# Performance work log

Measured on AMD Instinct MI355X. Metric: run time of the kernel, lower is better.

The kernel has to match this reference:

```python
import jax, jax.numpy as jnp
import numpy as np

B, S, D, H = 2, 2048, 1024, 16
DH = D // H  # 64


def setup_inputs() -> dict:
    key = jax.random.key(0)
    ks = jax.random.split(key, 9)
    s = 1.0 / np.sqrt(D)
    return {
        "x": jax.random.normal(ks[0], (B, S, D), dtype=jnp.float32),
        "Wq": jax.random.normal(ks[1], (D, D), dtype=jnp.float32) * s,
        "bq": jnp.zeros((D,), dtype=jnp.float32),
        "Wk": jax.random.normal(ks[2], (D, D), dtype=jnp.float32) * s,
        "bk": jnp.zeros((D,), dtype=jnp.float32),
        "Wv": jax.random.normal(ks[3], (D, D), dtype=jnp.float32) * s,
        "bv": jnp.zeros((D,), dtype=jnp.float32),
        "Wo": jax.random.normal(ks[4], (D, D), dtype=jnp.float32) * s,
        "bo": jnp.zeros((D,), dtype=jnp.float32),
    }


def _split_heads(t):
    # [B, S, D] -> [B, H, S, DH]
    return t.reshape(B, S, H, DH).transpose(0, 2, 1, 3)


def reference(x, Wq, bq, Wk, bk, Wv, bv, Wo, bo):
    q = _split_heads(x @ Wq + bq)
    k = _split_heads(x @ Wk + bk)
    v = _split_heads(x @ Wv + bv)
    scale = 1.0 / jnp.sqrt(jnp.asarray(DH, dtype=x.dtype))
    # [B, H, S, S] score matrix (materialized, as in the original)
    logits = jnp.einsum("bhqd,bhkd->bhqk", q, k) * scale
    attn = jax.nn.softmax(logits, axis=-1)
    out = jnp.einsum("bhqk,bhkd->bhqd", attn, v)
    out = out.transpose(0, 2, 1, 3).reshape(B, S, D)
    return out @ Wo + bo
```

## Files before the change

kernel.cpp:

```cpp
#include <hip/hip_runtime.h>
#include <hip/hip_bf16.h>
#include <stdint.h>


typedef __attribute__((ext_vector_type(8))) short bf16x8;
typedef __attribute__((ext_vector_type(4))) float f32x4;

__device__ __forceinline__ void gld16(const void* g, void* l) {
  __builtin_amdgcn_global_load_lds((const __attribute__((address_space(1))) void*)g,
                                   (__attribute__((address_space(3))) void*)l, 16, 0, 0);
}

__device__ __forceinline__ unsigned short f2b(float f) {
  __hip_bfloat16 h = __float2bfloat16(f);
  return *reinterpret_cast<unsigned short*>(&h);
}

__global__ __launch_bounds__(256) void prep_kernel(const float* __restrict__ x,
                                                   const float* __restrict__ Wq,
                                                   const float* __restrict__ Wk,
                                                   const float* __restrict__ Wv,
                                                   const float* __restrict__ Wo,
                                                   unsigned short* __restrict__ xb,
                                                   unsigned short* __restrict__ wt) {
  __shared__ unsigned short Ls[64 * 72];
  int bid = blockIdx.x;
  int t = threadIdx.x;
  if (bid < 4096) {
    int i = (bid * 256 + t) * 4;
    float4 v = *(const float4*)(x + i);
    ushort4 o = make_ushort4(f2b(v.x), f2b(v.y), f2b(v.z), f2b(v.w));
    *(ushort4*)(xb + i) = o;
    return;
  }
  int tid = bid - 4096;
  int z = tid >> 8, rem = tid & 255;
  int bx = rem & 15, by = rem >> 4;
  const float* src = (z == 0) ? Wq : (z == 1) ? Wk : (z == 2) ? Wv : Wo;
  unsigned short* dst = wt + (size_t)z * 1024 * 1024;
  int k0 = bx * 64, n0 = by * 64;
  int c4 = t & 15;
#pragma unroll
  for (int it = 0; it < 4; ++it) {
    int row = it * 16 + (t >> 4);
    float4 v = *(const float4*)(src + (k0 + row) * 1024 + n0 + c4 * 4);
    Ls[(c4 * 4 + 0) * 72 + row] = f2b(v.x);
    Ls[(c4 * 4 + 1) * 72 + row] = f2b(v.y);
    Ls[(c4 * 4 + 2) * 72 + row] = f2b(v.z);
    Ls[(c4 * 4 + 3) * 72 + row] = f2b(v.w);
  }
  __syncthreads();
  int nr = t >> 2, kc = (t & 3) * 16;
  *(uint4*)(dst + (size_t)(n0 + nr) * 1024 + k0 + kc) = *(uint4*)&Ls[nr * 72 + kc];
  *(uint4*)(dst + (size_t)(n0 + nr) * 1024 + k0 + kc + 8) = *(uint4*)&Ls[nr * 72 + kc + 8];
}

__global__ __launch_bounds__(256) void gemm_qkv(const unsigned short* __restrict__ Ab,
                                                const unsigned short* __restrict__ Bt,
                                                const float* __restrict__ bq,
                                                const float* __restrict__ bk,
                                                const float* __restrict__ bv,
                                                unsigned short* __restrict__ qb,
                                                unsigned short* __restrict__ kb,
                                                unsigned short* __restrict__ vtb) {
  __shared__ unsigned short As[128 * 32];
  __shared__ unsigned short Bs[128 * 32];
  __shared__ unsigned short Es[128 * 72];
  const int t = threadIdx.x;
  const int lane = t & 63, wave = t >> 6;
  const int m0 = blockIdx.x * 128, n0 = blockIdx.y * 128;
  const int wr = (wave >> 1) * 64, wc = (wave & 1) * 64;
  const int fr = lane & 15, fq = lane >> 4;
  f32x4 acc[4][4] = {};
  for (int kt = 0; kt < 32; ++kt) {
    const unsigned short* Ag = Ab + (size_t)m0 * 1024 + kt * 32;
    const unsigned short* Bg = Bt + (size_t)n0 * 1024 + kt * 32;
#pragma unroll
    for (int rep = 0; rep < 2; ++rep) {
      int c = t + rep * 256;
      int row = c >> 2, col = (c & 3) * 8;
      gld16(Ag + (size_t)row * 1024 + col, (void*)(As + c * 8));
      gld16(Bg + (size_t)row * 1024 + col, (void*)(Bs + c * 8));
    }
    __syncthreads();
    bf16x8 a[4], b[4];
#pragma unroll
    for (int i = 0; i < 4; ++i) a[i] = *(const bf16x8*)&As[(wr + i * 16 + fr) * 32 + fq * 8];
#pragma unroll
    for (int j = 0; j < 4; ++j) b[j] = *(const bf16x8*)&Bs[(wc + j * 16 + fr) * 32 + fq * 8];
#pragma unroll
    for (int i = 0; i < 4; ++i)
#pragma unroll
      for (int j = 0; j < 4; ++j)
        acc[i][j] = __builtin_amdgcn_mfma_f32_16x16x32_bf16(a[i], b[j], acc[i][j], 0, 0, 0);
    __syncthreads();
  }
  const int which = n0 >> 10;
  const int bidx = m0 >> 11, s0 = m0 & 2047;
  if (which == 2) {
#pragma unroll
    for (int nh = 0; nh < 2; ++nh) {
      if ((wc >> 6) == nh) {
#pragma unroll
        for (int j = 0; j < 4; ++j) {
          int col = j * 16 + fr;
          float bias = bv[(n0 + nh * 64 + col) & 1023];
#pragma unroll
          for (int i = 0; i < 4; ++i) {
            int sl = wr + i * 16 + fq * 4;
            ushort4 pk;
            pk.x = f2b(acc[i][j][0] + bias);
            pk.y = f2b(acc[i][j][1] + bias);
            pk.z = f2b(acc[i][j][2] + bias);
            pk.w = f2b(acc[i][j][3] + bias);
            *(uint2*)&Es[col * 136 + sl] = *(uint2*)&pk;
          }
        }
      }
      __syncthreads();
      int h = ((n0 + nh * 64) & 1023) >> 6;
#pragma unroll
      for (int it = 0; it < 4; ++it) {
        int dh = it * 16 + (t >> 4);
        int ck = (t & 15) * 8;
        uint4 vv = *(uint4*)&Es[dh * 136 + ck];
        *(uint4*)&vtb[(size_t)((bidx * 16 + h) * 64 + dh) * 2048 + s0 + ck] = vv;
      }
      __syncthreads();
    }
  } else {
    unsigned short* dst = (which == 0) ? qb : kb;
    const float* bias_p = (which == 0) ? bq : bk;
    float scale = (which == 0) ? 0.1803368801111204f : 1.0f;
#pragma unroll
    for (int nh = 0; nh < 2; ++nh) {
      if ((wc >> 6) == nh) {
#pragma unroll
        for (int j = 0; j < 4; ++j) {
          int col = j * 16 + fr;
          float bias = bias_p[(n0 + nh * 64 + col) & 1023];
#pragma unroll
          for (int i = 0; i < 4; ++i)
#pragma unroll
            for (int r = 0; r < 4; ++r) {
              int sl = wr + i * 16 + fq * 4 + r;
              Es[sl * 72 + col] = f2b((acc[i][j][r] + bias) * scale);
            }
        }
      }
      __syncthreads();
      int h = ((n0 + nh * 64) & 1023) >> 6;
#pragma unroll
      for (int it = 0; it < 4; ++it) {
        int sl = it * 32 + (t >> 3);
        int ck = (t & 7) * 8;
        uint4 vv = *(uint4*)&Es[sl * 72 + ck];
        *(uint4*)&dst[(size_t)((bidx * 16 + h) * 2048 + s0 + sl) * 64 + ck] = vv;
      }
      __syncthreads();
    }
  }
}

__global__ __launch_bounds__(256, 2) void attn_kernel(const unsigned short* __restrict__ qb,
                                                      const unsigned short* __restrict__ kb,
                                                      const unsigned short* __restrict__ vtb,
                                                      unsigned short* __restrict__ attn) {
  __shared__ unsigned short Ks[2 * 4096];
  __shared__ unsigned short Vs[2 * 4096];
  __shared__ unsigned short Ps[4 * 2048];
  const int t = threadIdx.x, lane = t & 63, w = t >> 6;
  const int fr = lane & 15, fq = lane >> 4;
  const int rid = blockIdx.y * 16 + blockIdx.x;
  const int bh = (rid & 7) + ((rid >> 7) << 3);
  const int q0 = ((rid >> 3) & 15) * 128;
  const int ksel = (fq ^ ((fr >> 1) & 3)) * 8;
  const unsigned short* qg = qb + (size_t)bh * 2048 * 64;
  const unsigned short* kg0 = kb + (size_t)bh * 2048 * 64;
  const unsigned short* vg0 = vtb + (size_t)bh * 64 * 2048;

  bf16x8 qf[2][2];
#pragma unroll
  for (int nb = 0; nb < 2; ++nb)
#pragma unroll
    for (int kk = 0; kk < 2; ++kk)
      qf[nb][kk] = *(const bf16x8*)(qg + (size_t)(q0 + w * 32 + nb * 16 + fr) * 64 + kk * 32 + fq * 8);

  bf16x8 ones;
#pragma unroll
  for (int i = 0; i < 8; ++i) ones[i] = (short)0x3F80;

  f32x4 oacc[2][4] = {};
  f32x4 lacc[2] = {};
  unsigned short* Pw = Ps + w * 2048;

  {
#pragma unroll
    for (int rep = 0; rep < 2; ++rep) {
      int c = t + rep * 256;
      int kk = c >> 8, row = (c >> 2) & 63, cc = c & 3;
      int cs = cc ^ ((row >> 1) & 3);
      gld16(kg0 + row * 64 + kk * 32 + cs * 8, (void*)(Ks + c * 8));
      gld16(vg0 + (size_t)row * 2048 + kk * 32 + cs * 8, (void*)(Vs + c * 8));
    }
  }

  for (int kt = 0; kt < 32; ++kt) {
    int buf = kt & 1;
    __syncthreads();
    if (kt + 1 < 32) {
      const unsigned short* kg = kg0 + (size_t)(kt + 1) * 4096;
      const unsigned short* vg = vg0 + (kt + 1) * 64;
      int lb = (buf ^ 1) * 4096;
#pragma unroll
      for (int rep = 0; rep < 2; ++rep) {
        int c = t + rep * 256;
        int kk = c >> 8, row = (c >> 2) & 63, cc = c & 3;
        int cs = cc ^ ((row >> 1) & 3);
        gld16(kg + row * 64 + kk * 32 + cs * 8, (void*)(Ks + lb + c * 8));
        gld16(vg + (size_t)row * 2048 + kk * 32 + cs * 8, (void*)(Vs + lb + c * 8));
      }
    }
    const unsigned short* Kb = Ks + buf * 4096;
    const unsigned short* Vb = Vs + buf * 4096;
    f32x4 sacc[4][2] = {};
#pragma unroll
    for (int kk = 0; kk < 2; ++kk) {
      bf16x8 kf[4];
#pragma unroll
      for (int m = 0; m < 4; ++m) kf[m] = *(const bf16x8*)&Kb[kk * 2048 + (m * 16 + fr) * 32 + ksel];
      __builtin_amdgcn_s_setprio(1);
#pragma unroll
      for (int m = 0; m < 4; ++m)
#pragma unroll
        for (int nb = 0; nb < 2; ++nb)
          sacc[m][nb] = __builtin_amdgcn_mfma_f32_16x16x32_bf16(kf[m], qf[nb][kk], sacc[m][nb], 0, 0, 0);
      __builtin_amdgcn_s_setprio(0);
    }
#pragma unroll
    for (int m = 0; m < 4; ++m)
#pragma unroll
      for (int nb = 0; nb < 2; ++nb) {
        int qw = nb * 16 + fr;
        int G = (m * 2 + (fq >> 1)) ^ (qw & 7);
        ushort4 pk;
        pk.x = f2b(__builtin_amdgcn_exp2f(sacc[m][nb][0]));
        pk.y = f2b(__builtin_amdgcn_exp2f(sacc[m][nb][1]));
        pk.z = f2b(__builtin_amdgcn_exp2f(sacc[m][nb][2]));
        pk.w = f2b(__builtin_amdgcn_exp2f(sacc[m][nb][3]));
        *(uint2*)&Pw[qw * 64 + G * 8 + (fq & 1) * 4] = *(uint2*)&pk;
      }
#pragma unroll
    for (int kk = 0; kk < 2; ++kk) {
      bf16x8 pf[2];
#pragma unroll
      for (int mb = 0; mb < 2; ++mb) {
        int qw = mb * 16 + fr;
        int G = (kk * 4 + fq) ^ (qw & 7);
        pf[mb] = *(const bf16x8*)&Pw[qw * 64 + G * 8];
      }
      __builtin_amdgcn_s_setprio(1);
#pragma unroll
      for (int n = 0; n < 4; ++n) {
        bf16x8 vf = *(const bf16x8*)&Vb[kk * 2048 + (n * 16 + fr) * 32 + ksel];
#pragma unroll
        for (int mb = 0; mb < 2; ++mb)
          oacc[mb][n] = __builtin_amdgcn_mfma_f32_16x16x32_bf16(pf[mb], vf, oacc[mb][n], 0, 0, 0);
      }
#pragma unroll
      for (int mb = 0; mb < 2; ++mb)
        lacc[mb] = __builtin_amdgcn_mfma_f32_16x16x32_bf16(pf[mb], ones, lacc[mb], 0, 0, 0);
      __builtin_amdgcn_s_setprio(0);
    }
  }
  int bidx = bh >> 4, h = bh & 15;
#pragma unroll
  for (int mb = 0; mb < 2; ++mb)
#pragma unroll
    for (int r = 0; r < 4; ++r) {
      float inv = 1.f / lacc[mb][r];
      int s = q0 + w * 32 + mb * 16 + fq * 4 + r;
      size_t base = (size_t)(bidx * 2048 + s) * 1024 + h * 64;
#pragma unroll
      for (int n = 0; n < 4; ++n) attn[base + n * 16 + fr] = f2b(oacc[mb][n][r] * inv);
    }
}

__global__ __launch_bounds__(256) void gemm_out(const unsigned short* __restrict__ Ab,
                                                const unsigned short* __restrict__ Bt,
                                                const float* __restrict__ bo,
                                                float* __restrict__ out) {
  __shared__ unsigned short As[128 * 32];
  __shared__ unsigned short Bs[64 * 32];
  const int t = threadIdx.x;
  const int lane = t & 63, wave = t >> 6;
  const int m0 = blockIdx.x * 128, n0 = blockIdx.y * 64;
  const int wr = (wave >> 1) * 64, wc = (wave & 1) * 32;
  const int fr = lane & 15, fq = lane >> 4;
  f32x4 acc[4][2] = {};
  for (int kt = 0; kt < 32; ++kt) {
    const unsigned short* Ag = Ab + (size_t)m0 * 1024 + kt * 32;
    const unsigned short* Bg = Bt + (size_t)n0 * 1024 + kt * 32;
#pragma unroll
    for (int rep = 0; rep < 2; ++rep) {
      int c = t + rep * 256;
      int row = c >> 2, col = (c & 3) * 8;
      gld16(Ag + (size_t)row * 1024 + col, (void*)(As + c * 8));
    }
    {
      int c = t;
      int row = c >> 2, col = (c & 3) * 8;
      gld16(Bg + (size_t)row * 1024 + col, (void*)(Bs + c * 8));
    }
    __syncthreads();
    bf16x8 a[4], b[2];
#pragma unroll
    for (int i = 0; i < 4; ++i) a[i] = *(const bf16x8*)&As[(wr + i * 16 + fr) * 32 + fq * 8];
#pragma unroll
    for (int j = 0; j < 2; ++j) b[j] = *(const bf16x8*)&Bs[(wc + j * 16 + fr) * 32 + fq * 8];
#pragma unroll
    for (int i = 0; i < 4; ++i)
#pragma unroll
      for (int j = 0; j < 2; ++j)
        acc[i][j] = __builtin_amdgcn_mfma_f32_16x16x32_bf16(a[i], b[j], acc[i][j], 0, 0, 0);
    __syncthreads();
  }
#pragma unroll
  for (int j = 0; j < 2; ++j) {
    int gn = n0 + wc + j * 16 + fr;
    float bias = bo[gn];
#pragma unroll
    for (int i = 0; i < 4; ++i)
#pragma unroll
      for (int r = 0; r < 4; ++r) {
        int gm = m0 + wr + i * 16 + fq * 4 + r;
        out[(size_t)gm * 1024 + gn] = acc[i][j][r] + bias;
      }
  }
}

extern "C" void kernel_launch(void* const* d_in, const int* in_sizes, int n_in,
                              void* d_out, int out_size, void* d_ws, size_t ws_size,
                              hipStream_t stream) {
  const float* x = (const float*)d_in[0];
  const float* Wq = (const float*)d_in[1];
  const float* bq = (const float*)d_in[2];
  const float* Wk = (const float*)d_in[3];
  const float* bk = (const float*)d_in[4];
  const float* Wv = (const float*)d_in[5];
  const float* bv = (const float*)d_in[6];
  const float* Wo = (const float*)d_in[7];
  const float* bo = (const float*)d_in[8];
  float* out = (float*)d_out;

  unsigned short* ws = (unsigned short*)d_ws;
  const size_t MI = (size_t)1024 * 1024;
  unsigned short* xb = ws;
  unsigned short* wt = ws + 4 * MI;
  unsigned short* qb = wt + 4 * MI;
  unsigned short* kb = qb + 4 * MI;
  unsigned short* vtb = kb + 4 * MI;
  unsigned short* attn = xb;

  prep_kernel<<<5120, 256, 0, stream>>>(x, Wq, Wk, Wv, Wo, xb, wt);
  gemm_qkv<<<dim3(32, 24), 256, 0, stream>>>(xb, wt, bq, bk, bv, qb, kb, vtb);
  attn_kernel<<<dim3(16, 32), 256, 0, stream>>>(qb, kb, vtb, attn);
  gemm_out<<<dim3(32, 16), 256, 0, stream>>>(attn, wt + 3 * MI, bo, out);
}
```

Measured before the change: 201.6 us.

## Software-pipeline attention loop with triple-buffered K/V and skewed QK/PV stages

Switches K/V shared memory from double to triple buffering and restructures the attention loop so each iteration computes QK^T for tile kt while doing the PV product for tile kt-1 from the previously written P buffer. The exp/bf16 conversion of scores is moved after the PV MFMAs so the exp work can overlap with the tensor ops. It adds a prologue and epilogue, keeps one barrier per iteration, and raises LDS use, which may lower occupancy at two blocks per CU.

```diff
diff --git a/kernel.cpp b/kernel.cpp
--- a/kernel.cpp
+++ b/kernel.cpp
@@ -166,8 +166,8 @@
                                                       const unsigned short* __restrict__ kb,
                                                       const unsigned short* __restrict__ vtb,
                                                       unsigned short* __restrict__ attn) {
-  __shared__ unsigned short Ks[2 * 4096];
-  __shared__ unsigned short Vs[2 * 4096];
+  __shared__ unsigned short Ks[3 * 4096];
+  __shared__ unsigned short Vs[3 * 4096];
   __shared__ unsigned short Ps[4 * 2048];
   const int t = threadIdx.x, lane = t & 63, w = t >> 6;
   const int fr = lane & 15, fq = lane >> 4;
@@ -194,41 +194,30 @@
   f32x4 lacc[2] = {};
   unsigned short* Pw = Ps + w * 2048;
 
-  {
+  auto STAGE = [&](int ktile, int slot) {
+    const unsigned short* kg = kg0 + (size_t)ktile * 4096;
+    const unsigned short* vg = vg0 + ktile * 64;
+    int lb = slot * 4096;
 #pragma unroll
     for (int rep = 0; rep < 2; ++rep) {
       int c = t + rep * 256;
       int kk = c >> 8, row = (c >> 2) & 63, cc = c & 3;
       int cs = cc ^ ((row >> 1) & 3);
-      gld16(kg0 + row * 64 + kk * 32 + cs * 8, (void*)(Ks + c * 8));
-      gld16(vg0 + (size_t)row * 2048 + kk * 32 + cs * 8, (void*)(Vs + c * 8));
-    }
-  }
-
-  for (int kt = 0; kt < 32; ++kt) {
-    int buf = kt & 1;
-    __syncthreads();
-    if (kt + 1 < 32) {
-      const unsigned short* kg = kg0 + (size_t)(kt + 1) * 4096;
-      const unsigned short* vg = vg0 + (kt + 1) * 64;
-      int lb = (buf ^ 1) * 4096;
-#pragma unroll
-      for (int rep = 0; rep < 2; ++rep) {
-        int c = t + rep * 256;
-        int kk = c >> 8, row = (c >> 2) & 63, cc = c & 3;
-        int cs = cc ^ ((row >> 1) & 3);
-        gld16(kg + row * 64 + kk * 32 + cs * 8, (void*)(Ks + lb + c * 8));
-        gld16(vg + (size_t)row * 2048 + kk * 32 + cs * 8, (void*)(Vs + lb + c * 8));
-      }
-    }
-    const unsigned short* Kb = Ks + buf * 4096;
-    const unsigned short* Vb = Vs + buf * 4096;
+      gld16(kg + row * 64 + kk * 32 + cs * 8, (void*)(Ks + lb + c * 8));
+      gld16(vg + (size_t)row * 2048 + kk * 32 + cs * 8, (void*)(Vs + lb + c * 8));
+    }
+  };
+
+  STAGE(0, 0);
+  __syncthreads();
+  STAGE(1, 1);
+  {
     f32x4 sacc[4][2] = {};
 #pragma unroll
     for (int kk = 0; kk < 2; ++kk) {
       bf16x8 kf[4];
 #pragma unroll
-      for (int m = 0; m < 4; ++m) kf[m] = *(const bf16x8*)&Kb[kk * 2048 + (m * 16 + fr) * 32 + ksel];
+      for (int m = 0; m < 4; ++m) kf[m] = *(const bf16x8*)&Ks[kk * 2048 + (m * 16 + fr) * 32 + ksel];
       __builtin_amdgcn_s_setprio(1);
 #pragma unroll
       for (int m = 0; m < 4; ++m)
@@ -250,6 +239,68 @@
         pk.w = f2b(__builtin_amdgcn_exp2f(sacc[m][nb][3]));
         *(uint2*)&Pw[qw * 64 + G * 8 + (fq & 1) * 4] = *(uint2*)&pk;
       }
+  }
+  __syncthreads();
+  STAGE(2, 2);
+
+  int prev = 0, cur = 1, nxt = 2;
+  for (int kt = 1; kt < 32; ++kt) {
+    const unsigned short* Kb = Ks + cur * 4096;
+    const unsigned short* Vb = Vs + prev * 4096;
+    f32x4 sacc[4][2] = {};
+    __builtin_amdgcn_s_setprio(1);
+#pragma unroll
+    for (int kk = 0; kk < 2; ++kk) {
+      bf16x8 kf[4];
+#pragma unroll
+      for (int m = 0; m < 4; ++m) kf[m] = *(const bf16x8*)&Kb[kk * 2048 + (m * 16 + fr) * 32 + ksel];
+#pragma unroll
+      for (int m = 0; m < 4; ++m)
+#pragma unroll
+        for (int nb = 0; nb < 2; ++nb)
+          sacc[m][nb] = __builtin_amdgcn_mfma_f32_16x16x32_bf16(kf[m], qf[nb][kk], sacc[m][nb], 0, 0, 0);
+    }
+#pragma unroll
+    for (int kk = 0; kk < 2; ++kk) {
+      bf16x8 pf[2];
+#pragma unroll
+      for (int mb = 0; mb < 2; ++mb) {
+        int qw = mb * 16 + fr;
+        int G = (kk * 4 + fq) ^ (qw & 7);
+        pf[mb] = *(const bf16x8*)&Pw[qw * 64 + G * 8];
+      }
+#pragma unroll
+      for (int n = 0; n < 4; ++n) {
+        bf16x8 vf = *(const bf16x8*)&Vb[kk * 2048 + (n * 16 + fr) * 32 + ksel];
+#pragma unroll
+        for (int mb = 0; mb < 2; ++mb)
+          oacc[mb][n] = __builtin_amdgcn_mfma_f32_16x16x32_bf16(pf[mb], vf, oacc[mb][n], 0, 0, 0);
+      }
+#pragma unroll
+      for (int mb = 0; mb < 2; ++mb)
+        lacc[mb] = __builtin_amdgcn_mfma_f32_16x16x32_bf16(pf[mb], ones, lacc[mb], 0, 0, 0);
+    }
+    __builtin_amdgcn_s_setprio(0);
+#pragma unroll
+    for (int m = 0; m < 4; ++m)
+#pragma unroll
+      for (int nb = 0; nb < 2; ++nb) {
+        int qw = nb * 16 + fr;
+        int G = (m * 2 + (fq >> 1)) ^ (qw & 7);
+        ushort4 pk;
+        pk.x = f2b(__builtin_amdgcn_exp2f(sacc[m][nb][0]));
+        pk.y = f2b(__builtin_amdgcn_exp2f(sacc[m][nb][1]));
+        pk.z = f2b(__builtin_amdgcn_exp2f(sacc[m][nb][2]));
+        pk.w = f2b(__builtin_amdgcn_exp2f(sacc[m][nb][3]));
+        *(uint2*)&Pw[qw * 64 + G * 8 + (fq & 1) * 4] = *(uint2*)&pk;
+      }
+    __syncthreads();
+    if (kt + 2 < 32) STAGE(kt + 2, prev);
+    int tmp = prev; prev = cur; cur = nxt; nxt = tmp;
+  }
+
+  {
+    const unsigned short* Vb = Vs + prev * 4096;
 #pragma unroll
     for (int kk = 0; kk < 2; ++kk) {
       bf16x8 pf[2];
```

New measurement: 199.3 us (median of 2 runs). About the same (-1.1%).
